# Performance work log

Measured on AMD Instinct MI355X. Metric: run time of the kernel, lower is better.

## Reference

```python
import jax, jax.numpy as jnp
import numpy as np

N_ENTS = 50000
N_RELS2 = 460  # num_rels * 2
H_DIM = 128
T = 8
E = 200000
M = 400000
RRELU_SLOPE = (1.0 / 8.0 + 1.0 / 3.0) / 2.0  # F.rrelu eval mode
EPS = 1e-12


def l2norm(x):
    # F.normalize(x) along last dim
    return x / jnp.maximum(jnp.linalg.norm(x, axis=-1, keepdims=True), EPS)


def gru_cell(x, h, W_ih, W_hh, b_ih, b_hh):
    # torch.nn.GRUCell math
    gi = x @ W_ih.T + b_ih
    gh = h @ W_hh.T + b_hh
    i_r, i_z, i_n = jnp.split(gi, 3, axis=-1)
    h_r, h_z, h_n = jnp.split(gh, 3, axis=-1)
    r = jax.nn.sigmoid(i_r + h_r)
    z = jax.nn.sigmoid(i_z + h_z)
    n = jnp.tanh(i_n + r * h_n)
    return (1.0 - z) * n + z * h


def rrelu(x):
    return jnp.where(x >= 0, x, RRELU_SLOPE * x)


def setup_inputs() -> dict:
    key = jax.random.key(0)
    ks = jax.random.split(key, 12)
    src = jax.random.randint(ks[0], (T, E), 0, N_ENTS, dtype=jnp.int32)
    dst = jax.random.randint(ks[1], (T, E), 0, N_ENTS, dtype=jnp.int32)
    etype = jax.random.randint(ks[2], (T, E), 0, N_RELS2, dtype=jnp.int32)
    r_to_e_idx = jax.random.randint(ks[3], (T, M), 0, N_ENTS, dtype=jnp.int32)
    rel_seg = jax.random.randint(ks[4], (T, M), 0, N_RELS2, dtype=jnp.int32)
    s = 1.0 / np.sqrt(H_DIM)
    dynamic_emb = jax.random.normal(ks[5], (N_ENTS, H_DIM), jnp.float32)
    emb_rel = jax.random.normal(ks[6], (N_RELS2, H_DIM), jnp.float32) * s
    gru_W_ih = jax.random.uniform(ks[7], (3 * H_DIM, 2 * H_DIM), jnp.float32, -s, s)
    gru_W_hh = jax.random.uniform(ks[8], (3 * H_DIM, H_DIM), jnp.float32, -s, s)
    gru_b_ih = jnp.zeros((3 * H_DIM,), jnp.float32)
    gru_b_hh = jnp.zeros((3 * H_DIM,), jnp.float32)
    rgcn_W = jax.random.normal(ks[9], (2, H_DIM, H_DIM), jnp.float32) * s  # 2 hidden layers
    time_gate_weight = jax.random.normal(ks[10], (H_DIM, H_DIM), jnp.float32) * s
    time_gate_bias = jnp.zeros((H_DIM,), jnp.float32)
    return {
        "src": src, "dst": dst, "etype": etype,
        "r_to_e_idx": r_to_e_idx, "rel_seg": rel_seg,
        "dynamic_emb": dynamic_emb, "emb_rel": emb_rel,
        "gru_W_ih": gru_W_ih, "gru_W_hh": gru_W_hh,
        "gru_b_ih": gru_b_ih, "gru_b_hh": gru_b_hh,
        "rgcn_W": rgcn_W,
        "time_gate_weight": time_gate_weight, "time_gate_bias": time_gate_bias,
    }


def reference(src, dst, etype, r_to_e_idx, rel_seg, dynamic_emb, emb_rel,
              gru_W_ih, gru_W_hh, gru_b_ih, gru_b_hh, rgcn_W,
              time_gate_weight, time_gate_bias):
    h_init = l2norm(dynamic_emb)  # layer_norm=True path

    def step(carry, xs):
        h, h0 = carry
        src_t, dst_t, etype_t, rte_t, rseg_t = xs
        # --- relation evolution: mean of incident entity embeddings per relation ---
        temp_e = h[rte_t]  # [M, d]
        sums = jax.ops.segment_sum(temp_e, rseg_t, num_segments=N_RELS2)
        cnts = jax.ops.segment_sum(jnp.ones((M,), h.dtype), rseg_t, num_segments=N_RELS2)
        x_mean = jnp.where(cnts[:, None] > 0, sums / jnp.maximum(cnts[:, None], 1.0), 0.0)
        x_input = jnp.concatenate([emb_rel, x_mean], axis=1)  # [2R, 2d]
        h0 = l2norm(gru_cell(x_input, h0, gru_W_ih, gru_W_hh, gru_b_ih, gru_b_hh))
        # --- RGCN (UnionRGCNLayer x2): msg=(h[src]+r[etype])@W, sum agg, 1/indeg norm, rrelu ---
        deg = jax.ops.segment_sum(jnp.ones((E,), h.dtype), dst_t, num_segments=N_ENTS)
        norm = jnp.where(deg > 0, 1.0 / jnp.maximum(deg, 1.0), 0.0)  # [N]
        nh = h
        for l in range(2):
            msg = (nh[src_t] + h0[etype_t]) @ rgcn_W[l]  # [E, d]
            agg = jax.ops.segment_sum(msg, dst_t, num_segments=N_ENTS) * norm[:, None]
            nh = rrelu(agg)
        current_h = l2norm(nh)
        # --- time gate fusion ---
        tw = jax.nn.sigmoid(h @ time_gate_weight + time_gate_bias)
        h_new = tw * current_h + (1.0 - tw) * h
        return (h_new, h0), h_new

    (_, h0_final), history = jax.lax.scan(
        step, (h_init, emb_rel), (src, dst, etype, r_to_e_idx, rel_seg))
    return history, h0_final  # [T, N, d], [2R, d]
```

## Files before the change

kernel.cpp:

```cpp
#include <hip/hip_runtime.h>
#include <math.h>

#define NENT 50000
#define NR2 460
#define HD 128
#define TS 8
#define EPC 200000
#define MPC 400000
#define RSLOPE 0.22916666666666666f
#define RBLK 128
#define NTOT (TS * NENT)
#define NB8 ((NTOT + 255) / 256)
#define SCAN2_PER ((NB8 + 255) / 256)
#define RSP 8

typedef __attribute__((ext_vector_type(8))) short bfrag;
typedef __attribute__((ext_vector_type(4))) float facc;

__device__ __forceinline__ float sigm(float x) { return 1.0f / (1.0f + expf(-x)); }
__device__ __forceinline__ float rrelu_f(float x) { return x >= 0.0f ? x : RSLOPE * x; }
__device__ __forceinline__ unsigned short f2bf_rne(float x) {
  unsigned u = __float_as_uint(x);
  unsigned r = (u + 0x7FFFu + ((u >> 16) & 1u)) >> 16;
  return (unsigned short)r;
}
__device__ __forceinline__ float bf2f(unsigned short b) {
  return __uint_as_float(((unsigned)b) << 16);
}
__device__ __forceinline__ float bfLO(unsigned u) { return __uint_as_float(u << 16); }
__device__ __forceinline__ float bfHI(unsigned u) { return __uint_as_float(u & 0xFFFF0000u); }

__global__ __launch_bounds__(HD) void k_l2rows(const float* __restrict__ in,
                                               float* __restrict__ out,
                                               unsigned short* __restrict__ out_bf) {
  int r = blockIdx.x, j = threadIdx.x;
  __shared__ float red[HD];
  float v = in[(size_t)r * HD + j];
  red[j] = v * v;
  __syncthreads();
  for (int s = HD / 2; s > 0; s >>= 1) { if (j < s) red[j] += red[j + s]; __syncthreads(); }
  float rn = 1.0f / fmaxf(sqrtf(red[0]), 1e-12f);
  float o = v * rn;
  out[(size_t)r * HD + j] = o;
  out_bf[(size_t)r * HD + j] = f2bf_rne(o);
}

__global__ void k_hist(const int* __restrict__ idx, int* __restrict__ cnt,
                       int n, int per_t, int stride) {
  int i = blockIdx.x * blockDim.x + threadIdx.x;
  int gs = gridDim.x * blockDim.x;
  for (; i < n; i += gs) atomicAdd(&cnt[(i / per_t) * stride + idx[i]], 1);
}

__global__ __launch_bounds__(256) void k_histR2(const int* __restrict__ rseg,
                                                int* __restrict__ blkcnt) {
  __shared__ int h[NR2];
  int b = blockIdx.x, t = blockIdx.y, tid = threadIdx.x;
  for (int i = tid; i < NR2; i += 256) h[i] = 0;
  __syncthreads();
  const int* rs = rseg + (size_t)t * MPC;
  int chunk = (MPC + RBLK - 1) / RBLK;
  int m0 = b * chunk, m1 = min(MPC, m0 + chunk);
  for (int m = m0 + tid; m < m1; m += 256) atomicAdd(&h[rs[m]], 1);
  __syncthreads();
  for (int i = tid; i < NR2; i += 256) blkcnt[((size_t)(t * RBLK + b)) * NR2 + i] = h[i];
}

__global__ __launch_bounds__(256) void k_scanR2a(const int* __restrict__ blkcnt,
                                                 int* __restrict__ tot) {
  int idx = blockIdx.x * 256 + threadIdx.x;
  if (idx >= TS * NR2) return;
  int t = idx / NR2, r = idx - t * NR2;
  int s = 0;
  for (int b = 0; b < RBLK; ++b) s += blkcnt[((size_t)(t * RBLK + b)) * NR2 + r];
  tot[idx] = s;
}

__global__ __launch_bounds__(512) void k_scanR2b(const int* __restrict__ tot,
    int* __restrict__ offsR, float* __restrict__ invc) {
  __shared__ int s[TS * NR2];
  int tid = threadIdx.x;
  for (int i = tid; i < TS * NR2; i += 512) s[i] = tot[i];
  __syncthreads();
  if (tid < TS) {
    int acc = tid * MPC;
    for (int r = 0; r < NR2; ++r) { int c = s[tid * NR2 + r]; s[tid * NR2 + r] = acc; acc += c; }
  }
  __syncthreads();
  for (int i = tid; i < TS * NR2; i += 512) {
    offsR[i] = s[i];
    int c = tot[i];
    invc[i] = c > 0 ? 1.0f / (float)c : 0.0f;
  }
  if (tid == 0) offsR[TS * NR2] = TS * MPC;
}

__global__ __launch_bounds__(256) void k_scanR2c(int* __restrict__ blkcnt,
                                                 const int* __restrict__ offsR) {
  int gw = (blockIdx.x * blockDim.x + threadIdx.x) >> 6;
  int lane = threadIdx.x & 63;
  if (gw >= TS * NR2) return;
  int t = gw / NR2, r = gw - t * NR2;
  size_t i0 = ((size_t)(t * RBLK + lane * 2)) * NR2 + r;
  size_t i1 = ((size_t)(t * RBLK + lane * 2 + 1)) * NR2 + r;
  int v0 = blkcnt[i0], v1 = blkcnt[i1];
  int s = v0 + v1;
  int sc = s;
  #pragma unroll
  for (int o = 1; o < 64; o <<= 1) {
    int x = __shfl_up(sc, o, 64);
    if (lane >= o) sc += x;
  }
  int basev = offsR[gw] + (sc - s);
  blkcnt[i0] = basev;
  blkcnt[i1] = basev + v0;
}

__global__ __launch_bounds__(256) void k_scatterR2(const int* __restrict__ rte,
    const int* __restrict__ rseg, const int* __restrict__ blkbase,
    int* __restrict__ out) {
  __shared__ int cur[NR2];
  int b = blockIdx.x, t = blockIdx.y, tid = threadIdx.x;
  for (int i = tid; i < NR2; i += 256) cur[i] = blkbase[((size_t)(t * RBLK + b)) * NR2 + i];
  __syncthreads();
  const int* rs = rseg + (size_t)t * MPC;
  const int* re = rte + (size_t)t * MPC;
  int chunk = (MPC + RBLK - 1) / RBLK;
  int m0 = b * chunk, m1 = min(MPC, m0 + chunk);
  for (int m = m0 + tid; m < m1; m += 256) {
    int r = rs[m];
    int p = atomicAdd(&cur[r], 1);
    out[p] = re[m];
  }
}

__global__ __launch_bounds__(256) void k_scan1(const int* __restrict__ deg,
    int* __restrict__ offs, float* __restrict__ normv, int* __restrict__ bsum) {
  __shared__ int sd[256];
  int b = blockIdx.x, tid = threadIdx.x;
  int i = b * 256 + tid;
  int v = (i < NTOT) ? deg[i] : 0;
  sd[tid] = v;
  __syncthreads();
  for (int o = 1; o < 256; o <<= 1) {
    int x = (tid >= o) ? sd[tid - o] : 0;
    __syncthreads();
    sd[tid] += x;
    __syncthreads();
  }
  if (i < NTOT) {
    offs[i] = sd[tid] - v;
    normv[i] = v > 0 ? 1.0f / (float)v : 0.0f;
  }
  if (tid == 255) bsum[b] = sd[255];
}

__global__ __launch_bounds__(256) void k_scan2(int* __restrict__ bsum) {
  __shared__ int part[256];
  int tid = threadIdx.x;
  int base = tid * SCAN2_PER;
  int local[SCAN2_PER];
  int s = 0;
  #pragma unroll
  for (int k = 0; k < SCAN2_PER; ++k) {
    int v = (base + k < NB8) ? bsum[base + k] : 0;
    local[k] = s;
    s += v;
  }
  part[tid] = s;
  __syncthreads();
  for (int o = 1; o < 256; o <<= 1) {
    int x = (tid >= o) ? part[tid - o] : 0;
    __syncthreads();
    part[tid] += x;
    __syncthreads();
  }
  int pre = (tid > 0) ? part[tid - 1] : 0;
  #pragma unroll
  for (int k = 0; k < SCAN2_PER; ++k)
    if (base + k < NB8) bsum[base + k] = pre + local[k];
}

__global__ __launch_bounds__(256) void k_scan3(int* __restrict__ offs, int* __restrict__ cur,
                                               const int* __restrict__ bsum) {
  int b = blockIdx.x;
  int i = b * 256 + threadIdx.x;
  if (i < NTOT) {
    int o = offs[i] + bsum[b];
    offs[i] = o;
    cur[i] = o;
  }
  if (b == 0 && threadIdx.x == 0) offs[NTOT] = TS * EPC;
}

__global__ void k_scatterE(const int* __restrict__ src, const int* __restrict__ dst,
                           const int* __restrict__ ety, int* __restrict__ cur,
                           unsigned* __restrict__ se) {
  int i = blockIdx.x * blockDim.x + threadIdx.x;
  int gs = gridDim.x * blockDim.x;
  for (; i < TS * EPC; i += gs) {
    int t = i / EPC;
    int d = dst[i];
    int p = atomicAdd(&cur[t * NENT + d], 1);
    se[p] = ((unsigned)src[i] << 9) | (unsigned)ety[i];
  }
}

__global__ __launch_bounds__(256) void k_prepW(const float* __restrict__ W,
    unsigned short* __restrict__ hi, unsigned short* __restrict__ lo) {
  int t = blockIdx.x * 256 + threadIdx.x;
  int nt = t >> 8, ks = (t >> 6) & 3, lane = t & 63;
  int n = nt * 16 + (lane & 15);
  int k0 = ks * 32 + ((lane >> 4) << 3);
  #pragma unroll
  for (int j = 0; j < 8; ++j) {
    float v = W[(k0 + j) * HD + n];
    unsigned short h = f2bf_rne(v);
    hi[t * 8 + j] = h;
    lo[t * 8 + j] = f2bf_rne(v - bf2f(h));
  }
}

__global__ __launch_bounds__(256) void k_relmean(const unsigned short* __restrict__ h_bf,
    const int* __restrict__ offs, const int* __restrict__ rte_csr,
    float* __restrict__ partials) {
  int rel = blockIdx.x, sp = blockIdx.y;
  int o0 = offs[rel], o1 = offs[rel + 1];
  int n = o1 - o0;
  int s0 = o0 + ((n * sp) >> 3);
  int s1 = o0 + ((n * (sp + 1)) >> 3);
  int w = threadIdx.x >> 6, lane = threadIdx.x & 63;
  const unsigned* h4 = (const unsigned*)h_bf;
  float sx = 0.f, sy = 0.f;
  int p = s0 + w;
  for (; p + 4 < s1; p += 8) {
    int i0 = rte_csr[p];
    int i1 = rte_csr[p + 4];
    unsigned u0 = h4[(size_t)i0 * 64 + lane];
    unsigned u1 = h4[(size_t)i1 * 64 + lane];
    sx += bfLO(u0) + bfLO(u1);
    sy += bfHI(u0) + bfHI(u1);
  }
  for (; p < s1; p += 4) {
    int i0 = rte_csr[p];
    unsigned u0 = h4[(size_t)i0 * 64 + lane];
    sx += bfLO(u0);
    sy += bfHI(u0);
  }
  __shared__ float red[4][HD];
  red[w][lane * 2] = sx;
  red[w][lane * 2 + 1] = sy;
  __syncthreads();
  if (threadIdx.x < HD) {
    int j = threadIdx.x;
    float t = red[0][j] + red[1][j] + red[2][j] + red[3][j];
    partials[((size_t)sp * NR2 + rel) * HD + j] = t;
  }
}

__global__ __launch_bounds__(HD) void k_gru(
    const float* __restrict__ partials, const float* __restrict__ invcnt,
    const float* __restrict__ emb_rel, const float* __restrict__ h0s,
    const float* __restrict__ Wih, const float* __restrict__ Whh,
    const float* __restrict__ bih, const float* __restrict__ bhh,
    float* __restrict__ h0d) {
  int r = blockIdx.x, j = threadIdx.x;
  __shared__ __align__(16) float xr[2 * HD];
  __shared__ __align__(16) float hh[HD];
  __shared__ float red[HD];
  float inv = invcnt[r];
  xr[j] = emb_rel[r * HD + j];
  float xm = 0.f;
  #pragma unroll
  for (int sp = 0; sp < RSP; ++sp) xm += partials[((size_t)sp * NR2 + r) * HD + j];
  xr[HD + j] = xm * inv;
  float hv0 = h0s[r * HD + j];
  hh[j] = hv0;
  __syncthreads();
  float gr = bih[j], gz = bih[HD + j], gn = bih[2 * HD + j];
  const float4* W4 = (const float4*)Wih;
  int rowA = j * 64, rowB = (j + HD) * 64, rowC = (j + 2 * HD) * 64;
  #pragma unroll 4
  for (int k4 = 0; k4 < 64; ++k4) {
    float4 xa = ((const float4*)xr)[k4];
    float4 w0 = W4[rowA + k4];
    float4 w1 = W4[rowB + k4];
    float4 w2 = W4[rowC + k4];
    gr += w0.x * xa.x + w0.y * xa.y + w0.z * xa.z + w0.w * xa.w;
    gz += w1.x * xa.x + w1.y * xa.y + w1.z * xa.z + w1.w * xa.w;
    gn += w2.x * xa.x + w2.y * xa.y + w2.z * xa.z + w2.w * xa.w;
  }
  float hr = bhh[j], hz = bhh[HD + j], hn = bhh[2 * HD + j];
  const float4* Wh4 = (const float4*)Whh;
  int rA = j * 32, rB = (j + HD) * 32, rC = (j + 2 * HD) * 32;
  #pragma unroll 4
  for (int k4 = 0; k4 < 32; ++k4) {
    float4 xa = ((const float4*)hh)[k4];
    float4 w0 = Wh4[rA + k4];
    float4 w1 = Wh4[rB + k4];
    float4 w2 = Wh4[rC + k4];
    hr += w0.x * xa.x + w0.y * xa.y + w0.z * xa.z + w0.w * xa.w;
    hz += w1.x * xa.x + w1.y * xa.y + w1.z * xa.z + w1.w * xa.w;
    hn += w2.x * xa.x + w2.y * xa.y + w2.z * xa.z + w2.w * xa.w;
  }
  float rg = sigm(gr + hr);
  float zg = sigm(gz + hz);
  float ng = tanhf(gn + rg * hn);
  float hv = (1.0f - zg) * ng + zg * hv0;
  red[j] = hv * hv;
  __syncthreads();
  for (int s = HD / 2; s > 0; s >>= 1) { if (j < s) red[j] += red[j + s]; __syncthreads(); }
  float rn = 1.0f / fmaxf(sqrtf(red[0]), 1e-12f);
  h0d[r * HD + j] = hv * rn;
}

__global__ __launch_bounds__(256) void k_edge_csr(
    const unsigned short* __restrict__ nh_bf, const float* __restrict__ h0,
    const int* __restrict__ offs, const unsigned* __restrict__ se,
    const float* __restrict__ norm, float* __restrict__ agg) {
  int gw = (blockIdx.x * blockDim.x + threadIdx.x) >> 6;
  int lane = threadIdx.x & 63;
  if (gw >= NENT) return;
  int o0 = offs[gw], o1 = offs[gw + 1];
  const unsigned* nh4 = (const unsigned*)nh_bf;
  const float2* h02 = (const float2*)h0;
  float sx = 0.f, sy = 0.f;
  int p = o0;
  for (; p + 2 <= o1; p += 2) {
    unsigned e0 = se[p];
    unsigned e1 = se[p + 1];
    unsigned ua = nh4[(size_t)(e0 >> 9) * 64 + lane];
    float2 ra = h02[(size_t)(e0 & 511u) * 64 + lane];
    unsigned ub = nh4[(size_t)(e1 >> 9) * 64 + lane];
    float2 rb = h02[(size_t)(e1 & 511u) * 64 + lane];
    sx += (bfLO(ua) + ra.x) + (bfLO(ub) + rb.x);
    sy += (bfHI(ua) + ra.y) + (bfHI(ub) + rb.y);
  }
  if (p < o1) {
    unsigned e0 = se[p];
    unsigned ua = nh4[(size_t)(e0 >> 9) * 64 + lane];
    float2 ra = h02[(size_t)(e0 & 511u) * 64 + lane];
    sx += bfLO(ua) + ra.x;
    sy += bfHI(ua) + ra.y;
  }
  float nm = norm[gw];
  ((float2*)agg)[(size_t)gw * 64 + lane] = make_float2(sx * nm, sy * nm);
}

template<int OUT_BF>
__global__ __launch_bounds__(256) void k_mm_mfma(
    float* __restrict__ A, unsigned short* __restrict__ Abf,
    const unsigned short* __restrict__ wHi, const unsigned short* __restrict__ wLo,
    int nrows) {
  __shared__ __align__(16) unsigned short AsH[64 * 128];
  __shared__ __align__(16) unsigned short AsL[64 * 128];
  int tid = threadIdx.x;
  int base = blockIdx.x * 64;
  const float4* A4 = (const float4*)A;
  #pragma unroll
  for (int it = 0; it < 8; ++it) {
    int idx = tid + it * 256;
    int r = idx >> 5, c4 = idx & 31;
    int c0 = c4 * 4;
    float4 v = make_float4(0.f, 0.f, 0.f, 0.f);
    if (base + r < nrows) v = A4[(size_t)(base + r) * 32 + c4];
    int chunk = (c0 >> 3) ^ (r & 7);
    int p = r * 128 + chunk * 8 + (c0 & 7);
    unsigned short h0 = f2bf_rne(v.x), h1 = f2bf_rne(v.y);
    unsigned short h2 = f2bf_rne(v.z), h3 = f2bf_rne(v.w);
    ushort4 hv; hv.x = h0; hv.y = h1; hv.z = h2; hv.w = h3;
    *(ushort4*)&AsH[p] = hv;
    ushort4 lv;
    lv.x = f2bf_rne(v.x - bf2f(h0)); lv.y = f2bf_rne(v.y - bf2f(h1));
    lv.z = f2bf_rne(v.z - bf2f(h2)); lv.w = f2bf_rne(v.w - bf2f(h3));
    *(ushort4*)&AsL[p] = lv;
  }
  __syncthreads();
  int w = tid >> 6, lane = tid & 63;
  int lrow = lane & 15, lk = lane >> 4;
  facc acc[8];
  #pragma unroll
  for (int nt = 0; nt < 8; ++nt) acc[nt] = (facc){0.f, 0.f, 0.f, 0.f};
  int arow = w * 16 + lrow;
  #pragma unroll
  for (int ks = 0; ks < 4; ++ks) {
    int chunk = (ks * 4 + lk) ^ (arow & 7);
    int p = arow * 128 + chunk * 8;
    bfrag aH = *(const bfrag*)&AsH[p];
    bfrag aL = *(const bfrag*)&AsL[p];
    #pragma unroll
    for (int nt = 0; nt < 8; ++nt) {
      int fi = ((nt * 4 + ks) * 64 + lane) * 8;
      bfrag bH = *(const bfrag*)&wHi[fi];
      bfrag bL = *(const bfrag*)&wLo[fi];
      acc[nt] = __builtin_amdgcn_mfma_f32_16x16x32_bf16(aH, bH, acc[nt], 0, 0, 0);
      acc[nt] = __builtin_amdgcn_mfma_f32_16x16x32_bf16(aH, bL, acc[nt], 0, 0, 0);
      acc[nt] = __builtin_amdgcn_mfma_f32_16x16x32_bf16(aL, bH, acc[nt], 0, 0, 0);
    }
  }
  #pragma unroll
  for (int nt = 0; nt < 8; ++nt)
    #pragma unroll
    for (int r = 0; r < 4; ++r) {
      int row = base + w * 16 + lk * 4 + r;
      if (row < nrows) {
        float res = rrelu_f(acc[nt][r]);
        if (OUT_BF) Abf[(size_t)row * HD + nt * 16 + lrow] = f2bf_rne(res);
        else A[(size_t)row * HD + nt * 16 + lrow] = res;
      }
    }
}

__global__ __launch_bounds__(256) void k_final_mfma(
    const float* __restrict__ C, const float* __restrict__ Hin, float* __restrict__ Hout,
    unsigned short* __restrict__ Hout_bf,
    const unsigned short* __restrict__ wHi, const unsigned short* __restrict__ wLo,
    const float* __restrict__ bias, int nrows) {
  __shared__ __align__(16) unsigned short AsH[64 * 128];
  __shared__ __align__(16) unsigned short AsL[64 * 128];
  int tid = threadIdx.x;
  int base = blockIdx.x * 64;
  const float4* H4 = (const float4*)Hin;
  #pragma unroll
  for (int it = 0; it < 8; ++it) {
    int idx = tid + it * 256;
    int r = idx >> 5, c4 = idx & 31;
    int c0 = c4 * 4;
    float4 v = make_float4(0.f, 0.f, 0.f, 0.f);
    if (base + r < nrows) v = H4[(size_t)(base + r) * 32 + c4];
    int chunk = (c0 >> 3) ^ (r & 7);
    int p = r * 128 + chunk * 8 + (c0 & 7);
    unsigned short h0 = f2bf_rne(v.x), h1 = f2bf_rne(v.y);
    unsigned short h2 = f2bf_rne(v.z), h3 = f2bf_rne(v.w);
    ushort4 hv; hv.x = h0; hv.y = h1; hv.z = h2; hv.w = h3;
    *(ushort4*)&AsH[p] = hv;
    ushort4 lv;
    lv.x = f2bf_rne(v.x - bf2f(h0)); lv.y = f2bf_rne(v.y - bf2f(h1));
    lv.z = f2bf_rne(v.z - bf2f(h2)); lv.w = f2bf_rne(v.w - bf2f(h3));
    *(ushort4*)&AsL[p] = lv;
  }
  __syncthreads();
  int w = tid >> 6, lane = tid & 63;
  int lrow = lane & 15, lk = lane >> 4;
  facc acc[8];
  #pragma unroll
  for (int nt = 0; nt < 8; ++nt) acc[nt] = (facc){0.f, 0.f, 0.f, 0.f};
  int arow = w * 16 + lrow;
  #pragma unroll
  for (int ks = 0; ks < 4; ++ks) {
    int chunk = (ks * 4 + lk) ^ (arow & 7);
    int p = arow * 128 + chunk * 8;
    bfrag aH = *(const bfrag*)&AsH[p];
    bfrag aL = *(const bfrag*)&AsL[p];
    #pragma unroll
    for (int nt = 0; nt < 8; ++nt) {
      int fi = ((nt * 4 + ks) * 64 + lane) * 8;
      bfrag bH = *(const bfrag*)&wHi[fi];
      bfrag bL = *(const bfrag*)&wLo[fi];
      acc[nt] = __builtin_amdgcn_mfma_f32_16x16x32_bf16(aH, bH, acc[nt], 0, 0, 0);
      acc[nt] = __builtin_amdgcn_mfma_f32_16x16x32_bf16(aH, bL, acc[nt], 0, 0, 0);
      acc[nt] = __builtin_amdgcn_mfma_f32_16x16x32_bf16(aL, bH, acc[nt], 0, 0, 0);
    }
  }
  float cv[8][4];
  float ss[4] = {0.f, 0.f, 0.f, 0.f};
  #pragma unroll
  for (int r = 0; r < 4; ++r) {
    int row = base + w * 16 + lk * 4 + r;
    int rok = row < nrows;
    #pragma unroll
    for (int nt = 0; nt < 8; ++nt) {
      float x = rok ? C[(size_t)row * HD + nt * 16 + lrow] : 0.f;
      cv[nt][r] = x;
      ss[r] += x * x;
    }
  }
  #pragma unroll
  for (int r = 0; r < 4; ++r) {
    #pragma unroll
    for (int o = 1; o < 16; o <<= 1) ss[r] += __shfl_xor(ss[r], o, 64);
    ss[r] = 1.0f / fmaxf(sqrtf(ss[r]), 1e-12f);
  }
  #pragma unroll
  for (int r = 0; r < 4; ++r) {
    int row = base + w * 16 + lk * 4 + r;
    if (row >= nrows) continue;
    #pragma unroll
    for (int nt = 0; nt < 8; ++nt) {
      int col = nt * 16 + lrow;
      float hv = Hin[(size_t)row * HD + col];
      float tw = sigm(acc[nt][r] + bias[col]);
      float res = tw * (cv[nt][r] * ss[r]) + (1.0f - tw) * hv;
      Hout[(size_t)row * HD + col] = res;
      Hout_bf[(size_t)row * HD + col] = f2bf_rne(res);
    }
  }
}

extern "C" void kernel_launch(void* const* d_in, const int* in_sizes, int n_in,
                              void* d_out, int out_size, void* d_ws, size_t ws_size,
                              hipStream_t stream) {
  const int* src    = (const int*)d_in[0];
  const int* dst    = (const int*)d_in[1];
  const int* etype  = (const int*)d_in[2];
  const int* rte    = (const int*)d_in[3];
  const int* rseg   = (const int*)d_in[4];
  const float* dyn  = (const float*)d_in[5];
  const float* emb_rel = (const float*)d_in[6];
  const float* W_ih = (const float*)d_in[7];
  const float* W_hh = (const float*)d_in[8];
  const float* b_ih = (const float*)d_in[9];
  const float* b_hh = (const float*)d_in[10];
  const float* rgcnW = (const float*)d_in[11];
  const float* tgW  = (const float*)d_in[12];
  const float* tgB  = (const float*)d_in[13];
  float* out = (float*)d_out;
  (void)in_sizes; (void)n_in; (void)out_size; (void)ws_size;

  float* ws = (float*)d_ws;
  size_t off = 0;
  float* agg1    = ws + off; off += (size_t)NENT * HD;
  float* agg2    = ws + off; off += (size_t)NENT * HD;
  float* parts   = ws + off; off += (size_t)RSP * NR2 * HD;
  float* h0a     = ws + off; off += (size_t)NR2 * HD;
  float* h0b     = ws + off; off += (size_t)NR2 * HD;
  float* normv8  = ws + off; off += NTOT;
  float* invc8   = ws + off; off += TS * NR2;
  off = (off + 3) & ~(size_t)3;
  unsigned short* h_bf    = (unsigned short*)(ws + off); off += (size_t)NENT * HD / 2;
  unsigned short* agg1_bf = (unsigned short*)(ws + off); off += (size_t)NENT * HD / 2;
  unsigned short* wf = (unsigned short*)(ws + off);
  unsigned short* w1H = wf;            unsigned short* w1L = wf + 16384;
  unsigned short* w2H = wf + 32768;    unsigned short* w2L = wf + 49152;
  unsigned short* wtH = wf + 65536;    unsigned short* wtL = wf + 81920;
  off += (6 * 16384) / 2;
  unsigned* csr_se8 = (unsigned*)(ws + off); off += (size_t)TS * EPC;
  int* csr_rte8  = (int*)(ws + off);  off += (size_t)TS * MPC;
  int* degE8     = (int*)(ws + off);  off += NTOT;
  int* offsE8    = (int*)(ws + off);  off += NTOT + 2;
  int* curE8     = (int*)(ws + off);  off += NTOT;
  int* bsum      = (int*)(ws + off);  off += NB8;
  int* blkcntR8  = (int*)(ws + off);  off += (size_t)TS * RBLK * NR2;
  int* offsR8    = (int*)(ws + off);  off += TS * NR2 + 2;
  int* totR      = (int*)(ws + off);  off += TS * NR2;

  hipMemsetAsync(degE8, 0, (size_t)NTOT * sizeof(int), stream);
  k_hist<<<2048, 256, 0, stream>>>(dst, degE8, TS * EPC, EPC, NENT);
  k_scan1<<<NB8, 256, 0, stream>>>(degE8, offsE8, normv8, bsum);
  k_scan2<<<1, 256, 0, stream>>>(bsum);
  k_scan3<<<NB8, 256, 0, stream>>>(offsE8, curE8, bsum);
  k_scatterE<<<2048, 256, 0, stream>>>(src, dst, etype, curE8, csr_se8);
  k_histR2<<<dim3(RBLK, TS), 256, 0, stream>>>(rseg, blkcntR8);
  k_scanR2a<<<(TS * NR2 + 255) / 256, 256, 0, stream>>>(blkcntR8, totR);
  k_scanR2b<<<1, 512, 0, stream>>>(totR, offsR8, invc8);
  k_scanR2c<<<(TS * NR2 * 64 + 255) / 256, 256, 0, stream>>>(blkcntR8, offsR8);
  k_scatterR2<<<dim3(RBLK, TS), 256, 0, stream>>>(rte, rseg, blkcntR8, csr_rte8);
  k_prepW<<<8, 256, 0, stream>>>(rgcnW, w1H, w1L);
  k_prepW<<<8, 256, 0, stream>>>(rgcnW + HD * HD, w2H, w2L);
  k_prepW<<<8, 256, 0, stream>>>(tgW, wtH, wtL);

  k_l2rows<<<NENT, HD, 0, stream>>>(dyn, out, h_bf);

  float* h0bufs[2] = {h0a, h0b};
  for (int t = 0; t < TS; ++t) {
    const float* h = out + (size_t)(t == 0 ? 0 : (t - 1)) * NENT * HD;
    float* hout = out + (size_t)t * NENT * HD;
    const float* h0s = (t == 0) ? emb_rel : h0bufs[(t - 1) & 1];
    float* h0d = h0bufs[t & 1];

    k_relmean<<<dim3(NR2, RSP), 256, 0, stream>>>(h_bf, offsR8 + t * NR2, csr_rte8, parts);
    k_gru<<<NR2, HD, 0, stream>>>(parts, invc8 + t * NR2, emb_rel, h0s,
                                  W_ih, W_hh, b_ih, b_hh, h0d);

    k_edge_csr<<<(NENT * 64 + 255) / 256, 256, 0, stream>>>(
        h_bf, h0d, offsE8 + t * NENT, csr_se8, normv8 + t * NENT, agg1);
    k_mm_mfma<1><<<(NENT + 63) / 64, 256, 0, stream>>>(agg1, agg1_bf, w1H, w1L, NENT);
    k_edge_csr<<<(NENT * 64 + 255) / 256, 256, 0, stream>>>(
        agg1_bf, h0d, offsE8 + t * NENT, csr_se8, normv8 + t * NENT, agg2);
    k_mm_mfma<0><<<(NENT + 63) / 64, 256, 0, stream>>>(agg2, (unsigned short*)nullptr,
                                                       w2H, w2L, NENT);
    k_final_mfma<<<(NENT + 63) / 64, 256, 0, stream>>>(agg2, h, hout, h_bf,
                                                       wtH, wtL, tgB, NENT);
  }
  hipMemcpyAsync(out + (size_t)TS * NENT * HD, h0bufs[(TS - 1) & 1],
                 (size_t)NR2 * HD * sizeof(float), hipMemcpyDeviceToDevice, stream);
}
```

Measured before the change: 1.690 ms.

## Fuse edge aggregation with MFMA matmuls and relation mean with GRU

```diff
diff --git a/kernel.cpp b/kernel.cpp
--- a/kernel.cpp
+++ b/kernel.cpp
@@ -12,7 +12,6 @@
 #define NTOT (TS * NENT)
 #define NB8 ((NTOT + 255) / 256)
 #define SCAN2_PER ((NB8 + 255) / 256)
-#define RSP 8
 
 typedef __attribute__((ext_vector_type(8))) short bfrag;
 typedef __attribute__((ext_vector_type(4))) float facc;
@@ -221,278 +220,257 @@
   }
 }
 
-__global__ __launch_bounds__(256) void k_relmean(const unsigned short* __restrict__ h_bf,
+__global__ __launch_bounds__(512) void k_relgru(
+    const unsigned short* __restrict__ h_bf,
     const int* __restrict__ offs, const int* __restrict__ rte_csr,
-    float* __restrict__ partials) {
-  int rel = blockIdx.x, sp = blockIdx.y;
-  int o0 = offs[rel], o1 = offs[rel + 1];
-  int n = o1 - o0;
-  int s0 = o0 + ((n * sp) >> 3);
-  int s1 = o0 + ((n * (sp + 1)) >> 3);
-  int w = threadIdx.x >> 6, lane = threadIdx.x & 63;
-  const unsigned* h4 = (const unsigned*)h_bf;
-  float sx = 0.f, sy = 0.f;
-  int p = s0 + w;
-  for (; p + 4 < s1; p += 8) {
-    int i0 = rte_csr[p];
-    int i1 = rte_csr[p + 4];
-    unsigned u0 = h4[(size_t)i0 * 64 + lane];
-    unsigned u1 = h4[(size_t)i1 * 64 + lane];
-    sx += bfLO(u0) + bfLO(u1);
-    sy += bfHI(u0) + bfHI(u1);
-  }
-  for (; p < s1; p += 4) {
-    int i0 = rte_csr[p];
-    unsigned u0 = h4[(size_t)i0 * 64 + lane];
-    sx += bfLO(u0);
-    sy += bfHI(u0);
-  }
-  __shared__ float red[4][HD];
-  red[w][lane * 2] = sx;
-  red[w][lane * 2 + 1] = sy;
-  __syncthreads();
-  if (threadIdx.x < HD) {
-    int j = threadIdx.x;
-    float t = red[0][j] + red[1][j] + red[2][j] + red[3][j];
-    partials[((size_t)sp * NR2 + rel) * HD + j] = t;
-  }
-}
-
-__global__ __launch_bounds__(HD) void k_gru(
-    const float* __restrict__ partials, const float* __restrict__ invcnt,
+    const float* __restrict__ invcnt,
     const float* __restrict__ emb_rel, const float* __restrict__ h0s,
     const float* __restrict__ Wih, const float* __restrict__ Whh,
     const float* __restrict__ bih, const float* __restrict__ bhh,
     float* __restrict__ h0d) {
-  int r = blockIdx.x, j = threadIdx.x;
+  int rel = blockIdx.x;
+  int tid = threadIdx.x;
+  int w = tid >> 6, lane = tid & 63;
+  int o0 = offs[rel], o1 = offs[rel + 1];
+  int n = o1 - o0;
+  int s0 = o0 + ((n * w) >> 3);
+  int s1 = o0 + ((n * (w + 1)) >> 3);
+  const unsigned* h4 = (const unsigned*)h_bf;
+  float sx = 0.f, sy = 0.f;
+  int p = s0;
+  for (; p + 1 < s1; p += 2) {
+    unsigned u0 = h4[(size_t)rte_csr[p] * 64 + lane];
+    unsigned u1 = h4[(size_t)rte_csr[p + 1] * 64 + lane];
+    sx += bfLO(u0) + bfLO(u1);
+    sy += bfHI(u0) + bfHI(u1);
+  }
+  if (p < s1) {
+    unsigned u0 = h4[(size_t)rte_csr[p] * 64 + lane];
+    sx += bfLO(u0);
+    sy += bfHI(u0);
+  }
+  __shared__ float red[8][HD];
+  red[w][lane * 2] = sx;
+  red[w][lane * 2 + 1] = sy;
+  __syncthreads();
   __shared__ __align__(16) float xr[2 * HD];
   __shared__ __align__(16) float hh[HD];
-  __shared__ float red[HD];
-  float inv = invcnt[r];
-  xr[j] = emb_rel[r * HD + j];
-  float xm = 0.f;
-  #pragma unroll
-  for (int sp = 0; sp < RSP; ++sp) xm += partials[((size_t)sp * NR2 + r) * HD + j];
-  xr[HD + j] = xm * inv;
-  float hv0 = h0s[r * HD + j];
-  hh[j] = hv0;
-  __syncthreads();
-  float gr = bih[j], gz = bih[HD + j], gn = bih[2 * HD + j];
-  const float4* W4 = (const float4*)Wih;
-  int rowA = j * 64, rowB = (j + HD) * 64, rowC = (j + 2 * HD) * 64;
-  #pragma unroll 4
-  for (int k4 = 0; k4 < 64; ++k4) {
-    float4 xa = ((const float4*)xr)[k4];
-    float4 w0 = W4[rowA + k4];
-    float4 w1 = W4[rowB + k4];
-    float4 w2 = W4[rowC + k4];
-    gr += w0.x * xa.x + w0.y * xa.y + w0.z * xa.z + w0.w * xa.w;
-    gz += w1.x * xa.x + w1.y * xa.y + w1.z * xa.z + w1.w * xa.w;
-    gn += w2.x * xa.x + w2.y * xa.y + w2.z * xa.z + w2.w * xa.w;
-  }
-  float hr = bhh[j], hz = bhh[HD + j], hn = bhh[2 * HD + j];
-  const float4* Wh4 = (const float4*)Whh;
-  int rA = j * 32, rB = (j + HD) * 32, rC = (j + 2 * HD) * 32;
-  #pragma unroll 4
-  for (int k4 = 0; k4 < 32; ++k4) {
-    float4 xa = ((const float4*)hh)[k4];
-    float4 w0 = Wh4[rA + k4];
-    float4 w1 = Wh4[rB + k4];
-    float4 w2 = Wh4[rC + k4];
-    hr += w0.x * xa.x + w0.y * xa.y + w0.z * xa.z + w0.w * xa.w;
-    hz += w1.x * xa.x + w1.y * xa.y + w1.z * xa.z + w1.w * xa.w;
-    hn += w2.x * xa.x + w2.y * xa.y + w2.z * xa.z + w2.w * xa.w;
-  }
-  float rg = sigm(gr + hr);
-  float zg = sigm(gz + hz);
-  float ng = tanhf(gn + rg * hn);
-  float hv = (1.0f - zg) * ng + zg * hv0;
-  red[j] = hv * hv;
-  __syncthreads();
-  for (int s = HD / 2; s > 0; s >>= 1) { if (j < s) red[j] += red[j + s]; __syncthreads(); }
-  float rn = 1.0f / fmaxf(sqrtf(red[0]), 1e-12f);
-  h0d[r * HD + j] = hv * rn;
-}
-
-__global__ __launch_bounds__(256) void k_edge_csr(
+  __shared__ float red2[HD];
+  float hv0 = 0.f;
+  if (tid < HD) {
+    int j = tid;
+    float inv = invcnt[rel];
+    float xm = 0.f;
+    #pragma unroll
+    for (int sp = 0; sp < 8; ++sp) xm += red[sp][j];
+    xr[j] = emb_rel[rel * HD + j];
+    xr[HD + j] = xm * inv;
+    hv0 = h0s[rel * HD + j];
+    hh[j] = hv0;
+  }
+  __syncthreads();
+  float hv = 0.f;
+  if (tid < HD) {
+    int j = tid;
+    float gr = bih[j], gz = bih[HD + j], gn = bih[2 * HD + j];
+    const float4* W4 = (const float4*)Wih;
+    int rowA = j * 64, rowB = (j + HD) * 64, rowC = (j + 2 * HD) * 64;
+    #pragma unroll 4
+    for (int k4 = 0; k4 < 64; ++k4) {
+      float4 xa = ((const float4*)xr)[k4];
+      float4 w0 = W4[rowA + k4];
+      float4 w1 = W4[rowB + k4];
+      float4 w2 = W4[rowC + k4];
+      gr += w0.x * xa.x + w0.y * xa.y + w0.z * xa.z + w0.w * xa.w;
+      gz += w1.x * xa.x + w1.y * xa.y + w1.z * xa.z + w1.w * xa.w;
+      gn += w2.x * xa.x + w2.y * xa.y + w2.z * xa.z + w2.w * xa.w;
+    }
+    float hr = bhh[j], hz = bhh[HD + j], hn = bhh[2 * HD + j];
+    const float4* Wh4 = (const float4*)Whh;
+    int rA = j * 32, rB = (j + HD) * 32, rC = (j + 2 * HD) * 32;
+    #pragma unroll 4
+    for (int k4 = 0; k4 < 32; ++k4) {
+      float4 xa = ((const float4*)hh)[k4];
+      float4 w0 = Wh4[rA + k4];
+      float4 w1 = Wh4[rB + k4];
+      float4 w2 = Wh4[rC + k4];
+      hr += w0.x * xa.x + w0.y * xa.y + w0.z * xa.z + w0.w * xa.w;
+      hz += w1.x * xa.x + w1.y * xa.y + w1.z * xa.z + w1.w * xa.w;
+      hn += w2.x * xa.x + w2.y * xa.y + w2.z * xa.z + w2.w * xa.w;
+    }
+    float rg = sigm(gr + hr);
+    float zg = sigm(gz + hz);
+    float ng = tanhf(gn + rg * hn);
+    hv = (1.0f - zg) * ng + zg * hv0;
+    red2[tid] = hv * hv;
+  }
+  __syncthreads();
+  for (int s = HD / 2; s > 0; s >>= 1) {
+    if (tid < s) red2[tid] += red2[tid + s];
+    __syncthreads();
+  }
+  if (tid < HD) {
+    float rn = 1.0f / fmaxf(sqrtf(red2[0]), 1e-12f);
+    h0d[rel * HD + tid] = hv * rn;
+  }
+}
+
+template<int FINAL>
+__global__ __launch_bounds__(512) void k_edge_mm(
     const unsigned short* __restrict__ nh_bf, const float* __restrict__ h0,
     const int* __restrict__ offs, const unsigned* __restrict__ se,
-    const float* __restrict__ norm, float* __restrict__ agg) {
-  int gw = (blockIdx.x * blockDim.x + threadIdx.x) >> 6;
-  int lane = threadIdx.x & 63;
-  if (gw >= NENT) return;
-  int o0 = offs[gw], o1 = offs[gw + 1];
-  const unsigned* nh4 = (const unsigned*)nh_bf;
-  const float2* h02 = (const float2*)h0;
-  float sx = 0.f, sy = 0.f;
-  int p = o0;
-  for (; p + 2 <= o1; p += 2) {
-    unsigned e0 = se[p];
-    unsigned e1 = se[p + 1];
-    unsigned ua = nh4[(size_t)(e0 >> 9) * 64 + lane];
-    float2 ra = h02[(size_t)(e0 & 511u) * 64 + lane];
-    unsigned ub = nh4[(size_t)(e1 >> 9) * 64 + lane];
-    float2 rb = h02[(size_t)(e1 & 511u) * 64 + lane];
-    sx += (bfLO(ua) + ra.x) + (bfLO(ub) + rb.x);
-    sy += (bfHI(ua) + ra.y) + (bfHI(ub) + rb.y);
-  }
-  if (p < o1) {
-    unsigned e0 = se[p];
-    unsigned ua = nh4[(size_t)(e0 >> 9) * 64 + lane];
-    float2 ra = h02[(size_t)(e0 & 511u) * 64 + lane];
-    sx += bfLO(ua) + ra.x;
-    sy += bfHI(ua) + ra.y;
-  }
-  float nm = norm[gw];
-  ((float2*)agg)[(size_t)gw * 64 + lane] = make_float2(sx * nm, sy * nm);
-}
-
-template<int OUT_BF>
-__global__ __launch_bounds__(256) void k_mm_mfma(
-    float* __restrict__ A, unsigned short* __restrict__ Abf,
+    const float* __restrict__ norm,
     const unsigned short* __restrict__ wHi, const unsigned short* __restrict__ wLo,
-    int nrows) {
-  __shared__ __align__(16) unsigned short AsH[64 * 128];
-  __shared__ __align__(16) unsigned short AsL[64 * 128];
-  int tid = threadIdx.x;
-  int base = blockIdx.x * 64;
-  const float4* A4 = (const float4*)A;
-  #pragma unroll
-  for (int it = 0; it < 8; ++it) {
-    int idx = tid + it * 256;
-    int r = idx >> 5, c4 = idx & 31;
-    int c0 = c4 * 4;
-    float4 v = make_float4(0.f, 0.f, 0.f, 0.f);
-    if (base + r < nrows) v = A4[(size_t)(base + r) * 32 + c4];
-    int chunk = (c0 >> 3) ^ (r & 7);
-    int p = r * 128 + chunk * 8 + (c0 & 7);
-    unsigned short h0 = f2bf_rne(v.x), h1 = f2bf_rne(v.y);
-    unsigned short h2 = f2bf_rne(v.z), h3 = f2bf_rne(v.w);
-    ushort4 hv; hv.x = h0; hv.y = h1; hv.z = h2; hv.w = h3;
-    *(ushort4*)&AsH[p] = hv;
-    ushort4 lv;
-    lv.x = f2bf_rne(v.x - bf2f(h0)); lv.y = f2bf_rne(v.y - bf2f(h1));
-    lv.z = f2bf_rne(v.z - bf2f(h2)); lv.w = f2bf_rne(v.w - bf2f(h3));
-    *(ushort4*)&AsL[p] = lv;
-  }
-  __syncthreads();
-  int w = tid >> 6, lane = tid & 63;
-  int lrow = lane & 15, lk = lane >> 4;
-  facc acc[8];
-  #pragma unroll
-  for (int nt = 0; nt < 8; ++nt) acc[nt] = (facc){0.f, 0.f, 0.f, 0.f};
-  int arow = w * 16 + lrow;
-  #pragma unroll
-  for (int ks = 0; ks < 4; ++ks) {
-    int chunk = (ks * 4 + lk) ^ (arow & 7);
-    int p = arow * 128 + chunk * 8;
-    bfrag aH = *(const bfrag*)&AsH[p];
-    bfrag aL = *(const bfrag*)&AsL[p];
-    #pragma unroll
-    for (int nt = 0; nt < 8; ++nt) {
-      int fi = ((nt * 4 + ks) * 64 + lane) * 8;
-      bfrag bH = *(const bfrag*)&wHi[fi];
-      bfrag bL = *(const bfrag*)&wLo[fi];
-      acc[nt] = __builtin_amdgcn_mfma_f32_16x16x32_bf16(aH, bH, acc[nt], 0, 0, 0);
-      acc[nt] = __builtin_amdgcn_mfma_f32_16x16x32_bf16(aH, bL, acc[nt], 0, 0, 0);
-      acc[nt] = __builtin_amdgcn_mfma_f32_16x16x32_bf16(aL, bH, acc[nt], 0, 0, 0);
-    }
-  }
-  #pragma unroll
-  for (int nt = 0; nt < 8; ++nt)
-    #pragma unroll
-    for (int r = 0; r < 4; ++r) {
-      int row = base + w * 16 + lk * 4 + r;
-      if (row < nrows) {
-        float res = rrelu_f(acc[nt][r]);
-        if (OUT_BF) Abf[(size_t)row * HD + nt * 16 + lrow] = f2bf_rne(res);
-        else A[(size_t)row * HD + nt * 16 + lrow] = res;
-      }
-    }
-}
-
-__global__ __launch_bounds__(256) void k_final_mfma(
-    const float* __restrict__ C, const float* __restrict__ Hin, float* __restrict__ Hout,
+    unsigned short* __restrict__ Abf,
+    const float* __restrict__ Hin, float* __restrict__ Hout,
     unsigned short* __restrict__ Hout_bf,
-    const unsigned short* __restrict__ wHi, const unsigned short* __restrict__ wLo,
+    const unsigned short* __restrict__ wtHi, const unsigned short* __restrict__ wtLo,
     const float* __restrict__ bias, int nrows) {
   __shared__ __align__(16) unsigned short AsH[64 * 128];
   __shared__ __align__(16) unsigned short AsL[64 * 128];
   int tid = threadIdx.x;
+  int w = tid >> 6, lane = tid & 63;
   int base = blockIdx.x * 64;
+  const unsigned* nh4 = (const unsigned*)nh_bf;
+  const float2* h02 = (const float2*)h0;
+  #pragma unroll
+  for (int rr = 0; rr < 8; ++rr) {
+    int row = w * 8 + rr;
+    int grow = base + row;
+    float sx = 0.f, sy = 0.f;
+    if (grow < nrows) {
+      int o0 = offs[grow], o1 = offs[grow + 1];
+      int p = o0;
+      for (; p + 2 <= o1; p += 2) {
+        unsigned e0 = se[p], e1 = se[p + 1];
+        unsigned ua = nh4[(size_t)(e0 >> 9) * 64 + lane];
+        float2 ra = h02[(size_t)(e0 & 511u) * 64 + lane];
+        unsigned ub = nh4[(size_t)(e1 >> 9) * 64 + lane];
+        float2 rb = h02[(size_t)(e1 & 511u) * 64 + lane];
+        sx += (bfLO(ua) + ra.x) + (bfLO(ub) + rb.x);
+        sy += (bfHI(ua) + ra.y) + (bfHI(ub) + rb.y);
+      }
+      if (p < o1) {
+        unsigned e0 = se[p];
+        unsigned ua = nh4[(size_t)(e0 >> 9) * 64 + lane];
+        float2 ra = h02[(size_t)(e0 & 511u) * 64 + lane];
+        sx += bfLO(ua) + ra.x;
+        sy += bfHI(ua) + ra.y;
+      }
+      float nm = norm[grow];
+      sx *= nm; sy *= nm;
+    }
+    int chunk = (lane >> 2) ^ (row & 7);
+    int pos = row * 128 + chunk * 8 + 2 * (lane & 3);
+    unsigned short hx = f2bf_rne(sx), hy = f2bf_rne(sy);
+    *(unsigned*)&AsH[pos] = (unsigned)hx | ((unsigned)hy << 16);
+    unsigned short lx = f2bf_rne(sx - bf2f(hx)), ly = f2bf_rne(sy - bf2f(hy));
+    *(unsigned*)&AsL[pos] = (unsigned)lx | ((unsigned)ly << 16);
+  }
+  __syncthreads();
+  int lrow = lane & 15, lk = lane >> 4;
+  facc acc[8];
+  #pragma unroll
+  for (int nt = 0; nt < 8; ++nt) acc[nt] = (facc){0.f, 0.f, 0.f, 0.f};
+  if (w < 4) {
+    int arow = w * 16 + lrow;
+    #pragma unroll
+    for (int ks = 0; ks < 4; ++ks) {
+      int chunk = (ks * 4 + lk) ^ (arow & 7);
+      int p = arow * 128 + chunk * 8;
+      bfrag aH = *(const bfrag*)&AsH[p];
+      bfrag aL = *(const bfrag*)&AsL[p];
+      #pragma unroll
+      for (int nt = 0; nt < 8; ++nt) {
+        int fi = ((nt * 4 + ks) * 64 + lane) * 8;
+        bfrag bH = *(const bfrag*)&wHi[fi];
+        bfrag bL = *(const bfrag*)&wLo[fi];
+        acc[nt] = __builtin_amdgcn_mfma_f32_16x16x32_bf16(aH, bH, acc[nt], 0, 0, 0);
+        acc[nt] = __builtin_amdgcn_mfma_f32_16x16x32_bf16(aH, bL, acc[nt], 0, 0, 0);
+        acc[nt] = __builtin_amdgcn_mfma_f32_16x16x32_bf16(aL, bH, acc[nt], 0, 0, 0);
+      }
+    }
+    #pragma unroll
+    for (int nt = 0; nt < 8; ++nt)
+      #pragma unroll
+      for (int r = 0; r < 4; ++r) acc[nt][r] = rrelu_f(acc[nt][r]);
+  }
+  if (FINAL == 0) {
+    if (w < 4) {
+      #pragma unroll
+      for (int nt = 0; nt < 8; ++nt)
+        #pragma unroll
+        for (int r = 0; r < 4; ++r) {
+          int row = base + w * 16 + lk * 4 + r;
+          if (row < nrows) Abf[(size_t)row * HD + nt * 16 + lrow] = f2bf_rne(acc[nt][r]);
+        }
+    }
+    return;
+  }
+  __syncthreads();
   const float4* H4 = (const float4*)Hin;
   #pragma unroll
-  for (int it = 0; it < 8; ++it) {
-    int idx = tid + it * 256;
+  for (int it = 0; it < 4; ++it) {
+    int idx = tid + it * 512;
     int r = idx >> 5, c4 = idx & 31;
     int c0 = c4 * 4;
     float4 v = make_float4(0.f, 0.f, 0.f, 0.f);
     if (base + r < nrows) v = H4[(size_t)(base + r) * 32 + c4];
     int chunk = (c0 >> 3) ^ (r & 7);
     int p = r * 128 + chunk * 8 + (c0 & 7);
-    unsigned short h0 = f2bf_rne(v.x), h1 = f2bf_rne(v.y);
-    unsigned short h2 = f2bf_rne(v.z), h3 = f2bf_rne(v.w);
-    ushort4 hv; hv.x = h0; hv.y = h1; hv.z = h2; hv.w = h3;
-    *(ushort4*)&AsH[p] = hv;
-    ushort4 lv;
-    lv.x = f2bf_rne(v.x - bf2f(h0)); lv.y = f2bf_rne(v.y - bf2f(h1));
-    lv.z = f2bf_rne(v.z - bf2f(h2)); lv.w = f2bf_rne(v.w - bf2f(h3));
-    *(ushort4*)&AsL[p] = lv;
-  }
-  __syncthreads();
-  int w = tid >> 6, lane = tid & 63;
-  int lrow = lane & 15, lk = lane >> 4;
-  facc acc[8];
-  #pragma unroll
-  for (int nt = 0; nt < 8; ++nt) acc[nt] = (facc){0.f, 0.f, 0.f, 0.f};
-  int arow = w * 16 + lrow;
-  #pragma unroll
-  for (int ks = 0; ks < 4; ++ks) {
-    int chunk = (ks * 4 + lk) ^ (arow & 7);
-    int p = arow * 128 + chunk * 8;
-    bfrag aH = *(const bfrag*)&AsH[p];
-    bfrag aL = *(const bfrag*)&AsL[p];
-    #pragma unroll
-    for (int nt = 0; nt < 8; ++nt) {
-      int fi = ((nt * 4 + ks) * 64 + lane) * 8;
-      bfrag bH = *(const bfrag*)&wHi[fi];
-      bfrag bL = *(const bfrag*)&wLo[fi];
-      acc[nt] = __builtin_amdgcn_mfma_f32_16x16x32_bf16(aH, bH, acc[nt], 0, 0, 0);
-      acc[nt] = __builtin_amdgcn_mfma_f32_16x16x32_bf16(aH, bL, acc[nt], 0, 0, 0);
-      acc[nt] = __builtin_amdgcn_mfma_f32_16x16x32_bf16(aL, bH, acc[nt], 0, 0, 0);
-    }
-  }
-  float cv[8][4];
-  float ss[4] = {0.f, 0.f, 0.f, 0.f};
-  #pragma unroll
-  for (int r = 0; r < 4; ++r) {
-    int row = base + w * 16 + lk * 4 + r;
-    int rok = row < nrows;
-    #pragma unroll
-    for (int nt = 0; nt < 8; ++nt) {
-      float x = rok ? C[(size_t)row * HD + nt * 16 + lrow] : 0.f;
-      cv[nt][r] = x;
-      ss[r] += x * x;
-    }
-  }
-  #pragma unroll
-  for (int r = 0; r < 4; ++r) {
-    #pragma unroll
-    for (int o = 1; o < 16; o <<= 1) ss[r] += __shfl_xor(ss[r], o, 64);
-    ss[r] = 1.0f / fmaxf(sqrtf(ss[r]), 1e-12f);
-  }
-  #pragma unroll
-  for (int r = 0; r < 4; ++r) {
-    int row = base + w * 16 + lk * 4 + r;
-    if (row >= nrows) continue;
-    #pragma unroll
-    for (int nt = 0; nt < 8; ++nt) {
-      int col = nt * 16 + lrow;
-      float hv = Hin[(size_t)row * HD + col];
-      float tw = sigm(acc[nt][r] + bias[col]);
-      float res = tw * (cv[nt][r] * ss[r]) + (1.0f - tw) * hv;
-      Hout[(size_t)row * HD + col] = res;
-      Hout_bf[(size_t)row * HD + col] = f2bf_rne(res);
+    unsigned short h0v = f2bf_rne(v.x), h1v = f2bf_rne(v.y);
+    unsigned short h2v = f2bf_rne(v.z), h3v = f2bf_rne(v.w);
+    ushort4 hvv; hvv.x = h0v; hvv.y = h1v; hvv.z = h2v; hvv.w = h3v;
+    *(ushort4*)&AsH[p] = hvv;
+    ushort4 lvv;
+    lvv.x = f2bf_rne(v.x - bf2f(h0v)); lvv.y = f2bf_rne(v.y - bf2f(h1v));
+    lvv.z = f2bf_rne(v.z - bf2f(h2v)); lvv.w = f2bf_rne(v.w - bf2f(h3v));
+    *(ushort4*)&AsL[p] = lvv;
+  }
+  __syncthreads();
+  if (w < 4) {
+    facc acc2[8];
+    #pragma unroll
+    for (int nt = 0; nt < 8; ++nt) acc2[nt] = (facc){0.f, 0.f, 0.f, 0.f};
+    int arow = w * 16 + lrow;
+    #pragma unroll
+    for (int ks = 0; ks < 4; ++ks) {
+      int chunk = (ks * 4 + lk) ^ (arow & 7);
+      int p = arow * 128 + chunk * 8;
+      bfrag aH = *(const bfrag*)&AsH[p];
+      bfrag aL = *(const bfrag*)&AsL[p];
+      #pragma unroll
+      for (int nt = 0; nt < 8; ++nt) {
+        int fi = ((nt * 4 + ks) * 64 + lane) * 8;
+        bfrag bH = *(const bfrag*)&wtHi[fi];
+        bfrag bL = *(const bfrag*)&wtLo[fi];
+        acc2[nt] = __builtin_amdgcn_mfma_f32_16x16x32_bf16(aH, bH, acc2[nt], 0, 0, 0);
+        acc2[nt] = __builtin_amdgcn_mfma_f32_16x16x32_bf16(aH, bL, acc2[nt], 0, 0, 0);
+        acc2[nt] = __builtin_amdgcn_mfma_f32_16x16x32_bf16(aL, bH, acc2[nt], 0, 0, 0);
+      }
+    }
+    float ss[4] = {0.f, 0.f, 0.f, 0.f};
+    #pragma unroll
+    for (int r = 0; r < 4; ++r) {
+      #pragma unroll
+      for (int nt = 0; nt < 8; ++nt) ss[r] += acc[nt][r] * acc[nt][r];
+      #pragma unroll
+      for (int o = 1; o < 16; o <<= 1) ss[r] += __shfl_xor(ss[r], o, 64);
+      ss[r] = 1.0f / fmaxf(sqrtf(ss[r]), 1e-12f);
+    }
+    #pragma unroll
+    for (int r = 0; r < 4; ++r) {
+      int row = base + w * 16 + lk * 4 + r;
+      if (row >= nrows) continue;
+      #pragma unroll
+      for (int nt = 0; nt < 8; ++nt) {
+        int col = nt * 16 + lrow;
+        float hv = Hin[(size_t)row * HD + col];
+        float tw = sigm(acc2[nt][r] + bias[col]);
+        float res = tw * (acc[nt][r] * ss[r]) + (1.0f - tw) * hv;
+        Hout[(size_t)row * HD + col] = res;
+        Hout_bf[(size_t)row * HD + col] = f2bf_rne(res);
+      }
     }
   }
 }
@@ -519,9 +497,6 @@
 
   float* ws = (float*)d_ws;
   size_t off = 0;
-  float* agg1    = ws + off; off += (size_t)NENT * HD;
-  float* agg2    = ws + off; off += (size_t)NENT * HD;
-  float* parts   = ws + off; off += (size_t)RSP * NR2 * HD;
   float* h0a     = ws + off; off += (size_t)NR2 * HD;
   float* h0b     = ws + off; off += (size_t)NR2 * HD;
   float* normv8  = ws + off; off += NTOT;
@@ -561,6 +536,7 @@
 
   k_l2rows<<<NENT, HD, 0, stream>>>(dyn, out, h_bf);
 
+  const int NBLK = (NENT + 63) / 64;
   float* h0bufs[2] = {h0a, h0b};
   for (int t = 0; t < TS; ++t) {
     const float* h = out + (size_t)(t == 0 ? 0 : (t - 1)) * NENT * HD;
@@ -568,19 +544,19 @@
     const float* h0s = (t == 0) ? emb_rel : h0bufs[(t - 1) & 1];
     float* h0d = h0bufs[t & 1];
 
-    k_relmean<<<dim3(NR2, RSP), 256, 0, stream>>>(h_bf, offsR8 + t * NR2, csr_rte8, parts);
-    k_gru<<<NR2, HD, 0, stream>>>(parts, invc8 + t * NR2, emb_rel, h0s,
-                                  W_ih, W_hh, b_ih, b_hh, h0d);
-
-    k_edge_csr<<<(NENT * 64 + 255) / 256, 256, 0, stream>>>(
-        h_bf, h0d, offsE8 + t * NENT, csr_se8, normv8 + t * NENT, agg1);
-    k_mm_mfma<1><<<(NENT + 63) / 64, 256, 0, stream>>>(agg1, agg1_bf, w1H, w1L, NENT);
-    k_edge_csr<<<(NENT * 64 + 255) / 256, 256, 0, stream>>>(
-        agg1_bf, h0d, offsE8 + t * NENT, csr_se8, normv8 + t * NENT, agg2);
-    k_mm_mfma<0><<<(NENT + 63) / 64, 256, 0, stream>>>(agg2, (unsigned short*)nullptr,
-                                                       w2H, w2L, NENT);
-    k_final_mfma<<<(NENT + 63) / 64, 256, 0, stream>>>(agg2, h, hout, h_bf,
-                                                       wtH, wtL, tgB, NENT);
+    k_relgru<<<NR2, 512, 0, stream>>>(h_bf, offsR8 + t * NR2, csr_rte8,
+                                      invc8 + t * NR2, emb_rel, h0s,
+                                      W_ih, W_hh, b_ih, b_hh, h0d);
+    k_edge_mm<0><<<NBLK, 512, 0, stream>>>(
+        h_bf, h0d, offsE8 + t * NENT, csr_se8, normv8 + t * NENT,
+        w1H, w1L, agg1_bf,
+        (const float*)nullptr, (float*)nullptr, (unsigned short*)nullptr,
+        (const unsigned short*)nullptr, (const unsigned short*)nullptr,
+        (const float*)nullptr, NENT);
+    k_edge_mm<1><<<NBLK, 512, 0, stream>>>(
+        agg1_bf, h0d, offsE8 + t * NENT, csr_se8, normv8 + t * NENT,
+        w2H, w2L, (unsigned short*)nullptr,
+        h, hout, h_bf, wtH, wtL, tgB, NENT);
   }
   hipMemcpyAsync(out + (size_t)TS * NENT * HD, h0bufs[(TS - 1) & 1],
                  (size_t)NR2 * HD * sizeof(float), hipMemcpyDeviceToDevice, stream);
```

New measurement: 2.098 ms. 24.1% more time.
